# Kernel optimization log

Hardware: AMD Instinct MI355X
Metric: run time of the kernel (lower is better)

The kernel has to match this reference:

```python
import jax, jax.numpy as jnp
import numpy as np

D, H, C, T, B = 1024, 128, 256, 16, 8192


def setup_inputs() -> dict:
    key = jax.random.key(0)
    ks = jax.random.split(key, 7)
    s = 0.02
    return {
        "x": jax.random.normal(ks[0], (B, D), dtype=jnp.float32),
        "Wr": jax.random.normal(ks[1], (D, T), dtype=jnp.float32) * s,  # router weight (transposed vs torch)
        "br": jnp.zeros((T,), dtype=jnp.float32),
        "W1": jax.random.normal(ks[2], (T, D, H), dtype=jnp.float32) * s,  # per-task fc1
        "b1": jnp.zeros((T, H), dtype=jnp.float32),
        "W2": jax.random.normal(ks[3], (T, H, C), dtype=jnp.float32) * s,  # per-task fc2
        "b2": jnp.zeros((T, C), dtype=jnp.float32),
    }


def reference(x, Wr, br, W1, b1, W2, b2):
    # Router: softmax over tasks, [B, T]
    task_probs = jax.nn.softmax(x @ Wr + br, axis=1)
    # All task experts as one batched grouped-GEMM pass.
    h = jax.nn.relu(jnp.einsum("bd,tdh->tbh", x, W1) + b1[:, None, :])  # [T, B, H]
    preds = jnp.einsum("tbh,thc->tbc", h, W2) + b2[:, None, :]           # [T, B, C]
    # Weight each task's predictions by its routing probability.
    task_preds = preds * task_probs.T[:, :, None]                         # [T, B, C]
    return task_probs, task_preds
```

## Files before the change

kernel.cpp:

```cpp
#include <hip/hip_runtime.h>

using bf16x8 = __attribute__((ext_vector_type(8))) short;
using f32x4  = __attribute__((ext_vector_type(4))) float;

#define B_SZ 8192
#define D_SZ 1024
#define H_SZ 128
#define C_SZ 256
#define T_SZ 16

__device__ __forceinline__ unsigned short f2bf(float f) {
  unsigned int u = __float_as_uint(f);
  return (unsigned short)((u + 0x7fffu + ((u >> 16) & 1u)) >> 16);
}

__global__ __launch_bounds__(256) void cast_x_kernel(const float* __restrict__ src,
                                                     unsigned short* __restrict__ dst, int n4) {
  int i = blockIdx.x * 256 + threadIdx.x;
  const int stride = gridDim.x * 256;
  for (; i < n4; i += stride) {
    float4 v = ((const float4*)src)[i];
    ushort4 o;
    o.x = f2bf(v.x); o.y = f2bf(v.y); o.z = f2bf(v.z); o.w = f2bf(v.w);
    ((ushort4*)dst)[i] = o;
  }
}

__global__ __launch_bounds__(256) void transpose_cast_kernel(const float* __restrict__ src,
                                                             unsigned short* __restrict__ dst,
                                                             int R, int C, int cshift) {
  __shared__ float tile[32][257];
  const int t = blockIdx.y;
  const int r0 = blockIdx.x * 32;
  const float* s = src + ((size_t)t * R + r0) * C;
  const int n = 32 * C;
  for (int idx = threadIdx.x; idx < n; idx += 256)
    tile[idx >> cshift][idx & (C - 1)] = s[idx];
  __syncthreads();
  unsigned short* d = dst + (size_t)t * C * R + r0;
  for (int idx = threadIdx.x; idx < n; idx += 256) {
    int cc = idx >> 5, rr = idx & 31;
    d[(size_t)cc * R + rr] = f2bf(tile[rr][cc]);
  }
}

__global__ __launch_bounds__(256) void router_kernel(const float* __restrict__ x,
                                                     const float* __restrict__ Wr,
                                                     const float* __restrict__ br,
                                                     float* __restrict__ out0) {
  const int lane = threadIdx.x & 63;
  const int wid  = threadIdx.x >> 6;
  const int brow = blockIdx.x * 16 + wid * 4;
  float acc[4][16];
#pragma unroll
  for (int r = 0; r < 4; ++r)
#pragma unroll
    for (int tt = 0; tt < 16; ++tt) acc[r][tt] = 0.f;

  for (int it = 0; it < 16; ++it) {
    const int d = it * 64 + lane;
    const float4* w4 = (const float4*)(Wr + (size_t)d * 16);
    float4 wa = w4[0], wb = w4[1], wc = w4[2], wd = w4[3];
    const float wv[16] = {wa.x, wa.y, wa.z, wa.w, wb.x, wb.y, wb.z, wb.w,
                          wc.x, wc.y, wc.z, wc.w, wd.x, wd.y, wd.z, wd.w};
#pragma unroll
    for (int r = 0; r < 4; ++r) {
      const float xv = x[(size_t)(brow + r) * 1024 + d];
#pragma unroll
      for (int tt = 0; tt < 16; ++tt) acc[r][tt] += xv * wv[tt];
    }
  }
#pragma unroll
  for (int off = 32; off >= 1; off >>= 1) {
#pragma unroll
    for (int r = 0; r < 4; ++r)
#pragma unroll
      for (int tt = 0; tt < 16; ++tt) acc[r][tt] += __shfl_xor(acc[r][tt], off);
  }
  if (lane == 0) {
#pragma unroll
    for (int r = 0; r < 4; ++r) {
      float v[16]; float m = -1e30f;
#pragma unroll
      for (int tt = 0; tt < 16; ++tt) { v[tt] = acc[r][tt] + br[tt]; m = fmaxf(m, v[tt]); }
      float ssum = 0.f;
#pragma unroll
      for (int tt = 0; tt < 16; ++tt) { v[tt] = __expf(v[tt] - m); ssum += v[tt]; }
      const float inv = 1.0f / ssum;
      float4* o = (float4*)(out0 + (size_t)(brow + r) * 16);
      o[0] = make_float4(v[0] * inv, v[1] * inv, v[2] * inv, v[3] * inv);
      o[1] = make_float4(v[4] * inv, v[5] * inv, v[6] * inv, v[7] * inv);
      o[2] = make_float4(v[8] * inv, v[9] * inv, v[10] * inv, v[11] * inv);
      o[3] = make_float4(v[12] * inv, v[13] * inv, v[14] * inv, v[15] * inv);
    }
  }
}

#define SX_OFF 0
#define SW_OFF 16384
#define SH_OFF 32768

__global__ __launch_bounds__(512, 4) void expert_kernel(
    const unsigned short* __restrict__ xb, const unsigned short* __restrict__ w1b,
    const unsigned short* __restrict__ w2b, const float* __restrict__ b1,
    const float* __restrict__ b2, const float* __restrict__ probs,
    float* __restrict__ out1) {
  __shared__ __align__(16) char smem[65536];
  const int tid  = threadIdx.x;
  const int lane = tid & 63;
  const int w    = tid >> 6;
  const int l16  = lane & 15;
  const int l4   = lane >> 4;

  const int bid = blockIdx.x;
  const int lid = (bid & 7) * 128 + (bid >> 3);
  const int t   = lid & 15;
  const int b0  = (lid >> 4) * 128;

  const int wn = w >> 1;
  const int wm = w & 1;

  f32x4 acc1[2][4] = {};

  const unsigned int o0 = (unsigned int)w * 4096u + (unsigned int)lane * 16u;

  for (int kt = 0; kt < 16; ++kt) {
#pragma unroll
    for (int it = 0; it < 4; ++it) {
      const unsigned int o  = o0 + (unsigned int)it * 1024u;
      const unsigned int oo = o & 16383u;
      const unsigned int p  = oo ^ (((oo >> 7) & 7u) << 4);
      const int row = (int)(p >> 7);
      const int kk  = (int)((p & 127u) >> 1);
      const unsigned short* g = (o < 16384u)
          ? (xb  + (((size_t)(b0 + row)) << 10) + (kt * 64 + kk))
          : (w1b + (((size_t)(t * 128 + row)) << 10) + (kt * 64 + kk));
      __builtin_amdgcn_global_load_lds(
          (const __attribute__((address_space(1))) unsigned int*)g,
          (__attribute__((address_space(3))) unsigned int*)(smem + ((size_t)w * 4096 + (size_t)it * 1024)),
          16, 0, 0);
    }
    __syncthreads();
#pragma unroll
    for (int ks = 0; ks < 2; ++ks) {
      const int k0b = (ks * 32 + l4 * 8) * 2;
      bf16x8 aw[2], bx[4];
#pragma unroll
      for (int ni = 0; ni < 2; ++ni) {
        const int row = wn * 32 + ni * 16 + l16;
        const int byte = (row << 7) + k0b;
        aw[ni] = *(const bf16x8*)(smem + SW_OFF + (byte ^ ((row & 7) << 4)));
      }
#pragma unroll
      for (int mi = 0; mi < 4; ++mi) {
        const int row = wm * 64 + mi * 16 + l16;
        const int byte = (row << 7) + k0b;
        bx[mi] = *(const bf16x8*)(smem + SX_OFF + (byte ^ ((row & 7) << 4)));
      }
#pragma unroll
      for (int ni = 0; ni < 2; ++ni)
#pragma unroll
        for (int mi = 0; mi < 4; ++mi)
          acc1[ni][mi] = __builtin_amdgcn_mfma_f32_16x16x32_bf16(aw[ni], bx[mi], acc1[ni][mi], 0, 0, 0);
    }
    __syncthreads();
  }

#pragma unroll
  for (int ni = 0; ni < 2; ++ni) {
    const int n0 = wn * 32 + ni * 16 + l4 * 4;
    float bb[4];
#pragma unroll
    for (int r = 0; r < 4; ++r) bb[r] = b1[t * 128 + n0 + r];
#pragma unroll
    for (int mi = 0; mi < 4; ++mi) {
      const int m = wm * 64 + mi * 16 + l16;
      unsigned int pk[2];
#pragma unroll
      for (int h = 0; h < 2; ++h) {
        float v0 = fmaxf(acc1[ni][mi][2 * h + 0] + bb[2 * h + 0], 0.f);
        float v1 = fmaxf(acc1[ni][mi][2 * h + 1] + bb[2 * h + 1], 0.f);
        pk[h] = (unsigned int)f2bf(v0) | ((unsigned int)f2bf(v1) << 16);
      }
      int byte = (m << 8) + n0 * 2;
      byte ^= ((m & 7) << 4);
      *(uint2*)(smem + SH_OFF + byte) = make_uint2(pk[0], pk[1]);
    }
  }
  __syncthreads();

  const int wm2 = w >> 1;
  const int wc2 = w & 1;
  f32x4 acc2[2][8] = {};
  const unsigned short* w2t = w2b + (size_t)t * C_SZ * H_SZ;

#pragma unroll
  for (int ks = 0; ks < 4; ++ks) {
    const int k0 = ks * 32 + l4 * 8;
    bf16x8 ah[2];
#pragma unroll
    for (int mi = 0; mi < 2; ++mi) {
      const int row = wm2 * 32 + mi * 16 + l16;
      const int byte = (row << 8) + k0 * 2;
      ah[mi] = *(const bf16x8*)(smem + SH_OFF + (byte ^ ((row & 7) << 4)));
    }
#pragma unroll
    for (int ci = 0; ci < 8; ++ci) {
      const int c = wc2 * 128 + ci * 16 + l16;
      bf16x8 bw = *(const bf16x8*)(w2t + (size_t)c * 128 + k0);
#pragma unroll
      for (int mi = 0; mi < 2; ++mi)
        acc2[mi][ci] = __builtin_amdgcn_mfma_f32_16x16x32_bf16(ah[mi], bw, acc2[mi][ci], 0, 0, 0);
    }
  }

  const size_t outbase = (size_t)t * B_SZ * C_SZ;
#pragma unroll
  for (int mi = 0; mi < 2; ++mi) {
    const int mrow0 = wm2 * 32 + mi * 16 + l4 * 4;
    float pv[4];
#pragma unroll
    for (int r = 0; r < 4; ++r) pv[r] = probs[(size_t)(b0 + mrow0 + r) * 16 + t];
#pragma unroll
    for (int ci = 0; ci < 8; ++ci) {
      const int c = wc2 * 128 + ci * 16 + l16;
      const float bias = b2[t * 256 + c];
#pragma unroll
      for (int r = 0; r < 4; ++r)
        out1[outbase + (size_t)(b0 + mrow0 + r) * 256 + c] = (acc2[mi][ci][r] + bias) * pv[r];
    }
  }
}

extern "C" void kernel_launch(void* const* d_in, const int* in_sizes, int n_in,
                              void* d_out, int out_size, void* d_ws, size_t ws_size,
                              hipStream_t stream) {
  const float* x  = (const float*)d_in[0];
  const float* Wr = (const float*)d_in[1];
  const float* br = (const float*)d_in[2];
  const float* W1 = (const float*)d_in[3];
  const float* b1 = (const float*)d_in[4];
  const float* W2 = (const float*)d_in[5];
  const float* b2 = (const float*)d_in[6];
  float* out0 = (float*)d_out;
  float* out1 = out0 + (size_t)B_SZ * T_SZ;

  char* ws = (char*)d_ws;
  unsigned short* xb  = (unsigned short*)ws;
  unsigned short* w1b = (unsigned short*)(ws + (size_t)16777216);
  unsigned short* w2b = (unsigned short*)(ws + (size_t)16777216 + 4194304);

  cast_x_kernel<<<2048, 256, 0, stream>>>(x, xb, (B_SZ * D_SZ) / 4);
  transpose_cast_kernel<<<dim3(D_SZ / 32, T_SZ), 256, 0, stream>>>(W1, w1b, D_SZ, H_SZ, 7);
  transpose_cast_kernel<<<dim3(H_SZ / 32, T_SZ), 256, 0, stream>>>(W2, w2b, H_SZ, C_SZ, 8);
  router_kernel<<<B_SZ / 16, 256, 0, stream>>>(x, Wr, br, out0);
  expert_kernel<<<1024, 512, 0, stream>>>(xb, w1b, w2b, b1, b2, out0, out1);
}
```

Before: 121.6 us.

## Double-buffer fc1 loads and enlarge expert tile to 256 rows

The expert kernel now handles 256 batch rows per block instead of 128, so each W1 tile loaded into LDS is reused across twice as many rows. The fc1 K loop double-buffers the global-to-LDS copies: the next stage is issued before the current one is computed, which removes one barrier per iteration and overlaps memory with MFMA work. Per-thread accumulators grow (acc1 and acc2 each go to 4x4 and 4x8), LDS rises to 96KB and occupancy drops to 2 blocks per CU. The grid is halved to 512 blocks, which may leave parts of the GPU underused.

New measurement: 109.0 us. -10.3%, faster.

```diff
diff --git a/kernel.cpp b/kernel.cpp
--- a/kernel.cpp
+++ b/kernel.cpp
@@ -96,16 +96,14 @@
   }
 }
 
-#define SX_OFF 0
-#define SW_OFF 16384
-#define SH_OFF 32768
-
-__global__ __launch_bounds__(512, 4) void expert_kernel(
+#define SW_REG 65536
+
+__global__ __launch_bounds__(512, 2) void expert_kernel(
     const unsigned short* __restrict__ xb, const unsigned short* __restrict__ w1b,
     const unsigned short* __restrict__ w2b, const float* __restrict__ b1,
     const float* __restrict__ b2, const float* __restrict__ probs,
     float* __restrict__ out1) {
-  __shared__ __align__(16) char smem[65536];
+  __shared__ __align__(16) char smem[98304];
   const int tid  = threadIdx.x;
   const int lane = tid & 63;
   const int w    = tid >> 6;
@@ -113,62 +111,87 @@
   const int l4   = lane >> 4;
 
   const int bid = blockIdx.x;
-  const int lid = (bid & 7) * 128 + (bid >> 3);
+  const int lid = (bid & 7) * 64 + (bid >> 3);
   const int t   = lid & 15;
-  const int b0  = (lid >> 4) * 128;
-
-  const int wn = w >> 1;
-  const int wm = w & 1;
-
-  f32x4 acc1[2][4] = {};
-
-  const unsigned int o0 = (unsigned int)w * 4096u + (unsigned int)lane * 16u;
-
-  for (int kt = 0; kt < 16; ++kt) {
-#pragma unroll
-    for (int it = 0; it < 4; ++it) {
-      const unsigned int o  = o0 + (unsigned int)it * 1024u;
-      const unsigned int oo = o & 16383u;
-      const unsigned int p  = oo ^ (((oo >> 7) & 7u) << 4);
-      const int row = (int)(p >> 7);
-      const int kk  = (int)((p & 127u) >> 1);
-      const unsigned short* g = (o < 16384u)
-          ? (xb  + (((size_t)(b0 + row)) << 10) + (kt * 64 + kk))
-          : (w1b + (((size_t)(t * 128 + row)) << 10) + (kt * 64 + kk));
-      __builtin_amdgcn_global_load_lds(
-          (const __attribute__((address_space(1))) unsigned int*)g,
-          (__attribute__((address_space(3))) unsigned int*)(smem + ((size_t)w * 4096 + (size_t)it * 1024)),
-          16, 0, 0);
-    }
+  const int b0  = (lid >> 4) * 256;
+
+  const unsigned short* gp[6];
+  unsigned int ldo[6];
+#pragma unroll
+  for (int it = 0; it < 6; ++it) {
+    if (it < 4) {
+      const unsigned int o = (unsigned int)w * 4096u + (unsigned int)it * 1024u + (unsigned int)lane * 16u;
+      const int row = (int)(o >> 7);
+      const int cb  = (int)((o & 127u) ^ (((unsigned)row & 7u) << 4));
+      gp[it]  = xb + (size_t)(b0 + row) * 1024 + (cb >> 1);
+      ldo[it] = o;
+    } else {
+      const unsigned int o = (unsigned int)w * 2048u + (unsigned int)(it - 4) * 1024u + (unsigned int)lane * 16u;
+      const int row = (int)(o >> 7);
+      const int cb  = (int)((o & 127u) ^ (((unsigned)row & 7u) << 4));
+      gp[it]  = w1b + (size_t)(t * 128 + row) * 1024 + (cb >> 1);
+      ldo[it] = o;
+    }
+  }
+
+#define STAGE(curbuf, kt)                                                              \
+  {                                                                                    \
+    _Pragma("unroll")                                                                  \
+    for (int it = 0; it < 6; ++it) {                                                   \
+      const unsigned short* g = gp[it] + (kt) * 64;                                    \
+      char* dd = smem + (it < 4 ? (curbuf) * 32768 + (int)ldo[it]                      \
+                                : SW_REG + (curbuf) * 16384 + (int)ldo[it]);           \
+      __builtin_amdgcn_global_load_lds(                                                \
+          (const __attribute__((address_space(1))) unsigned int*)g,                    \
+          (__attribute__((address_space(3))) unsigned int*)dd, 16, 0, 0);              \
+    }                                                                                  \
+  }
+
+  const int wn = w & 1;
+  const int wm = w >> 1;
+  f32x4 acc1[4][4] = {};
+
+#define FC1_COMPUTE(curbuf)                                                            \
+  {                                                                                    \
+    const int bx_base = (curbuf) * 32768;                                              \
+    const int aw_base = SW_REG + (curbuf) * 16384;                                     \
+    _Pragma("unroll")                                                                  \
+    for (int ks = 0; ks < 2; ++ks) {                                                   \
+      const int cb = ks * 64 + l4 * 16;                                                \
+      bf16x8 aw[4], bx[4];                                                             \
+      _Pragma("unroll")                                                                \
+      for (int ni = 0; ni < 4; ++ni) {                                                 \
+        const int row = wn * 64 + ni * 16 + l16;                                       \
+        aw[ni] = *(const bf16x8*)(smem + aw_base + (row << 7) + (cb ^ ((row & 7) << 4)));\
+      }                                                                                \
+      _Pragma("unroll")                                                                \
+      for (int mi = 0; mi < 4; ++mi) {                                                 \
+        const int row = wm * 64 + mi * 16 + l16;                                       \
+        bx[mi] = *(const bf16x8*)(smem + bx_base + (row << 7) + (cb ^ ((row & 7) << 4)));\
+      }                                                                                \
+      _Pragma("unroll")                                                                \
+      for (int ni = 0; ni < 4; ++ni)                                                   \
+        _Pragma("unroll")                                                              \
+        for (int mi = 0; mi < 4; ++mi)                                                 \
+          acc1[ni][mi] = __builtin_amdgcn_mfma_f32_16x16x32_bf16(aw[ni], bx[mi], acc1[ni][mi], 0, 0, 0); \
+    }                                                                                  \
+  }
+
+  STAGE(0, 0);
+  __syncthreads();
+  int cur = 0;
+  for (int kt = 0; kt < 15; ++kt) {
+    STAGE(cur ^ 1, kt + 1);
+    FC1_COMPUTE(cur);
     __syncthreads();
-#pragma unroll
-    for (int ks = 0; ks < 2; ++ks) {
-      const int k0b = (ks * 32 + l4 * 8) * 2;
-      bf16x8 aw[2], bx[4];
-#pragma unroll
-      for (int ni = 0; ni < 2; ++ni) {
-        const int row = wn * 32 + ni * 16 + l16;
-        const int byte = (row << 7) + k0b;
-        aw[ni] = *(const bf16x8*)(smem + SW_OFF + (byte ^ ((row & 7) << 4)));
-      }
-#pragma unroll
-      for (int mi = 0; mi < 4; ++mi) {
-        const int row = wm * 64 + mi * 16 + l16;
-        const int byte = (row << 7) + k0b;
-        bx[mi] = *(const bf16x8*)(smem + SX_OFF + (byte ^ ((row & 7) << 4)));
-      }
-#pragma unroll
-      for (int ni = 0; ni < 2; ++ni)
-#pragma unroll
-        for (int mi = 0; mi < 4; ++mi)
-          acc1[ni][mi] = __builtin_amdgcn_mfma_f32_16x16x32_bf16(aw[ni], bx[mi], acc1[ni][mi], 0, 0, 0);
-    }
-    __syncthreads();
-  }
-
-#pragma unroll
-  for (int ni = 0; ni < 2; ++ni) {
-    const int n0 = wn * 32 + ni * 16 + l4 * 4;
+    cur ^= 1;
+  }
+  FC1_COMPUTE(cur);
+  __syncthreads();
+
+#pragma unroll
+  for (int ni = 0; ni < 4; ++ni) {
+    const int n0 = wn * 64 + ni * 16 + l4 * 4;
     float bb[4];
 #pragma unroll
     for (int r = 0; r < 4; ++r) bb[r] = b1[t * 128 + n0 + r];
@@ -182,52 +205,50 @@
         float v1 = fmaxf(acc1[ni][mi][2 * h + 1] + bb[2 * h + 1], 0.f);
         pk[h] = (unsigned int)f2bf(v0) | ((unsigned int)f2bf(v1) << 16);
       }
-      int byte = (m << 8) + n0 * 2;
-      byte ^= ((m & 7) << 4);
-      *(uint2*)(smem + SH_OFF + byte) = make_uint2(pk[0], pk[1]);
+      const int byte = (m << 8) + ((n0 * 2) ^ ((m & 7) << 4));
+      *(uint2*)(smem + byte) = make_uint2(pk[0], pk[1]);
     }
   }
   __syncthreads();
 
   const int wm2 = w >> 1;
-  const int wc2 = w & 1;
-  f32x4 acc2[2][8] = {};
+  const int wc  = w & 1;
+  f32x4 acc2[4][8] = {};
   const unsigned short* w2t = w2b + (size_t)t * C_SZ * H_SZ;
 
 #pragma unroll
   for (int ks = 0; ks < 4; ++ks) {
-    const int k0 = ks * 32 + l4 * 8;
-    bf16x8 ah[2];
-#pragma unroll
-    for (int mi = 0; mi < 2; ++mi) {
-      const int row = wm2 * 32 + mi * 16 + l16;
-      const int byte = (row << 8) + k0 * 2;
-      ah[mi] = *(const bf16x8*)(smem + SH_OFF + (byte ^ ((row & 7) << 4)));
+    const int cb = ks * 64 + l4 * 16;
+    bf16x8 ah[4];
+#pragma unroll
+    for (int mi = 0; mi < 4; ++mi) {
+      const int row = wm2 * 64 + mi * 16 + l16;
+      ah[mi] = *(const bf16x8*)(smem + (row << 8) + (cb ^ ((row & 7) << 4)));
     }
 #pragma unroll
     for (int ci = 0; ci < 8; ++ci) {
-      const int c = wc2 * 128 + ci * 16 + l16;
-      bf16x8 bw = *(const bf16x8*)(w2t + (size_t)c * 128 + k0);
-#pragma unroll
-      for (int mi = 0; mi < 2; ++mi)
+      const int c = wc * 128 + ci * 16 + l16;
+      bf16x8 bw = *(const bf16x8*)(w2t + (size_t)c * 128 + ks * 32 + l4 * 8);
+#pragma unroll
+      for (int mi = 0; mi < 4; ++mi)
         acc2[mi][ci] = __builtin_amdgcn_mfma_f32_16x16x32_bf16(ah[mi], bw, acc2[mi][ci], 0, 0, 0);
     }
   }
 
-  const size_t outbase = (size_t)t * B_SZ * C_SZ;
-#pragma unroll
-  for (int mi = 0; mi < 2; ++mi) {
-    const int mrow0 = wm2 * 32 + mi * 16 + l4 * 4;
+  const size_t outbase = (size_t)t * (size_t)(B_SZ * C_SZ);
+#pragma unroll
+  for (int mi = 0; mi < 4; ++mi) {
+    const int m0 = wm2 * 64 + mi * 16 + l4 * 4;
     float pv[4];
 #pragma unroll
-    for (int r = 0; r < 4; ++r) pv[r] = probs[(size_t)(b0 + mrow0 + r) * 16 + t];
+    for (int r = 0; r < 4; ++r) pv[r] = probs[(size_t)(b0 + m0 + r) * 16 + t];
 #pragma unroll
     for (int ci = 0; ci < 8; ++ci) {
-      const int c = wc2 * 128 + ci * 16 + l16;
+      const int c = wc * 128 + ci * 16 + l16;
       const float bias = b2[t * 256 + c];
 #pragma unroll
       for (int r = 0; r < 4; ++r)
-        out1[outbase + (size_t)(b0 + mrow0 + r) * 256 + c] = (acc2[mi][ci][r] + bias) * pv[r];
+        out1[outbase + (size_t)(b0 + m0 + r) * 256 + c] = (acc2[mi][ci][r] + bias) * pv[r];
     }
   }
 }
@@ -254,5 +275,5 @@
   transpose_cast_kernel<<<dim3(D_SZ / 32, T_SZ), 256, 0, stream>>>(W1, w1b, D_SZ, H_SZ, 7);
   transpose_cast_kernel<<<dim3(H_SZ / 32, T_SZ), 256, 0, stream>>>(W2, w2b, H_SZ, C_SZ, 8);
   router_kernel<<<B_SZ / 16, 256, 0, stream>>>(x, Wr, br, out0);
-  expert_kernel<<<1024, 512, 0, stream>>>(xb, w1b, w2b, b1, b2, out0, out1);
-}
+  expert_kernel<<<512, 512, 0, stream>>>(xb, w1b, w2b, b1, b2, out0, out1);
+}
```
